# Kernel optimization log

Measured on AMD Instinct MI355X. Metric: run time of the kernel, lower is better.

Reference implementation:

```python
import jax, jax.numpy as jnp
import numpy as np

D = 1024      # num_embd
H = 16        # num_heads
HD = D // H   # head_size = 64
DFF = 4 * D
EPS = 1e-5


def layernorm(x, g, b):
    mu = jnp.mean(x, axis=-1, keepdims=True)
    var = jnp.mean((x - mu) ** 2, axis=-1, keepdims=True)
    return (x - mu) * jax.lax.rsqrt(var + EPS) * g + b


def setup_inputs() -> dict:
    key = jax.random.key(0)
    ks = jax.random.split(key, 12)
    B, S = 2, 2048
    s = lambda d: 1.0 / np.sqrt(d)
    return {
        "x": jax.random.normal(ks[0], (B, S, D), jnp.float32),
        "Wq": jax.random.normal(ks[1], (H, D, HD), jnp.float32) * s(D),
        "Wk": jax.random.normal(ks[2], (H, D, HD), jnp.float32) * s(D),
        "Wv": jax.random.normal(ks[3], (H, D, HD), jnp.float32) * s(D),
        "Wp": jax.random.normal(ks[4], (D, D), jnp.float32) * s(D),
        "bp": jnp.zeros((D,), jnp.float32),
        "W1": jax.random.normal(ks[5], (D, DFF), jnp.float32) * s(D),
        "b1": jnp.zeros((DFF,), jnp.float32),
        "W2": jax.random.normal(ks[6], (DFF, D), jnp.float32) * s(DFF),
        "b2": jnp.zeros((D,), jnp.float32),
        "g1": jnp.ones((D,), jnp.float32),
        "beta1": jnp.zeros((D,), jnp.float32),
        "g2": jnp.ones((D,), jnp.float32),
        "beta2": jnp.zeros((D,), jnp.float32),
    }


def reference(x, Wq, Wk, Wv, Wp, bp, W1, b1, W2, b2, g1, beta1, g2, beta2):
    B, S, _ = x.shape
    # --- self-attention with pre-LN residual ---
    h = layernorm(x, g1, beta1)
    q = jnp.einsum('bsd,hdk->bhsk', h, Wq)
    k = jnp.einsum('bsd,hdk->bhsk', h, Wk)
    v = jnp.einsum('bsd,hdk->bhsk', h, Wv)
    scores = jnp.einsum('bhqk,bhsk->bhqs', q, k) * (HD ** -0.5)
    causal = jnp.tril(jnp.ones((S, S), bool))
    scores = jnp.where(causal, scores, -jnp.inf)
    att = jax.nn.softmax(scores, axis=-1)          # dropout=0.0 (eval)
    o = jnp.einsum('bhqs,bhsk->bhqk', att, v)
    o = o.transpose(0, 2, 1, 3).reshape(B, S, D)   # concat heads
    x = x + o @ Wp + bp
    # --- feed-forward with pre-LN residual ---
    h2 = layernorm(x, g2, beta2)
    x = x + jax.nn.relu(h2 @ W1 + b1) @ W2 + b2
    return x
```

## Files before the change

### kernel.cpp

```cpp
#include <hip/hip_runtime.h>
#include <math.h>

#define DMODEL 1024
#define NHEAD  16
#define HD     64
#define DFF    4096
#define SEQ    2048
#define BATCH  2
#define NTOK   (BATCH * SEQ)
#define LN_EPS 1e-5f

typedef __attribute__((ext_vector_type(8))) short short8;
typedef __attribute__((ext_vector_type(4))) float floatx4;
typedef __attribute__((ext_vector_type(4))) unsigned short ushort4v;

__device__ __forceinline__ unsigned short f2bf(float x) {
  unsigned int u = __float_as_uint(x);
  return (unsigned short)((u + 0x7FFFu + ((u >> 16) & 1u)) >> 16);
}
__device__ __forceinline__ float bf2f(unsigned short h) {
  return __uint_as_float(((unsigned int)h) << 16);
}
__device__ __forceinline__ void split2(float x, unsigned short& hi, unsigned short& lo) {
  hi = f2bf(x);
  lo = f2bf(x - bf2f(hi));
}

__global__ __launch_bounds__(256) void ln_split(
    const float* __restrict__ x, const float* __restrict__ g,
    const float* __restrict__ beta, short* __restrict__ ohi,
    short* __restrict__ olo) {
  int row = blockIdx.x;
  const float4* xr = (const float4*)(x + (size_t)row * DMODEL);
  float4 v = xr[threadIdx.x];
  float s  = v.x + v.y + v.z + v.w;
  float sq = v.x * v.x + v.y * v.y + v.z * v.z + v.w * v.w;
#pragma unroll
  for (int off = 1; off < 64; off <<= 1) {
    s  += __shfl_xor(s, off);
    sq += __shfl_xor(sq, off);
  }
  __shared__ float red_s[4], red_q[4];
  int wave = threadIdx.x >> 6, lane = threadIdx.x & 63;
  if (lane == 0) { red_s[wave] = s; red_q[wave] = sq; }
  __syncthreads();
  s  = red_s[0] + red_s[1] + red_s[2] + red_s[3];
  sq = red_q[0] + red_q[1] + red_q[2] + red_q[3];
  float mu  = s * (1.0f / DMODEL);
  float var = sq * (1.0f / DMODEL) - mu * mu;
  float r   = rsqrtf(var + LN_EPS);
  float4 gv = ((const float4*)g)[threadIdx.x];
  float4 bv = ((const float4*)beta)[threadIdx.x];
  float o0 = (v.x - mu) * r * gv.x + bv.x;
  float o1 = (v.y - mu) * r * gv.y + bv.y;
  float o2 = (v.z - mu) * r * gv.z + bv.z;
  float o3 = (v.w - mu) * r * gv.w + bv.w;
  ushort4v hi, lo;
  unsigned short h_, l_;
  split2(o0, h_, l_); hi.x = h_; lo.x = l_;
  split2(o1, h_, l_); hi.y = h_; lo.y = l_;
  split2(o2, h_, l_); hi.z = h_; lo.z = l_;
  split2(o3, h_, l_); hi.w = h_; lo.w = l_;
  size_t base = (size_t)row * DMODEL + threadIdx.x * 4;
  *(ushort4v*)(ohi + base) = hi;
  *(ushort4v*)(olo + base) = lo;
}

__global__ __launch_bounds__(256) void split_rows(
    const float* __restrict__ in, short* __restrict__ ohi,
    short* __restrict__ olo) {
  size_t i = ((size_t)blockIdx.x * 256 + threadIdx.x) * 4;
  float4 v = *(const float4*)(in + i);
  ushort4v hi, lo;
  unsigned short h_, l_;
  split2(v.x, h_, l_); hi.x = h_; lo.x = l_;
  split2(v.y, h_, l_); hi.y = h_; lo.y = l_;
  split2(v.z, h_, l_); hi.z = h_; lo.z = l_;
  split2(v.w, h_, l_); hi.w = h_; lo.w = l_;
  *(ushort4v*)(ohi + i) = hi;
  *(ushort4v*)(olo + i) = lo;
}

__global__ __launch_bounds__(256) void repack_qkvT(
    const float* __restrict__ Wq, const float* __restrict__ Wk,
    const float* __restrict__ Wv, short* __restrict__ ohi,
    short* __restrict__ olo) {
  int i = blockIdx.x * 256 + threadIdx.x;
  int col = i >> 10;
  int d   = i & 1023;
  int m   = col >> 10;
  int c   = col & 1023;
  const float* W = (m == 0) ? Wq : (m == 1 ? Wk : Wv);
  int hh = c >> 6, kk = c & 63;
  float w = W[((size_t)hh * DMODEL + d) * HD + kk];
  unsigned short h_, l_;
  split2(w, h_, l_);
  ohi[i] = (short)h_;
  olo[i] = (short)l_;
}

__global__ __launch_bounds__(256) void transpose_split(
    const float* __restrict__ in, short* __restrict__ ohi,
    short* __restrict__ olo, int lgR, int C) {
  int i = blockIdx.x * 256 + threadIdx.x;
  int R = 1 << lgR;
  int oc = i >> lgR;
  int orow = i & (R - 1);
  float w = in[(size_t)orow * C + oc];
  unsigned short h_, l_;
  split2(w, h_, l_);
  ohi[i] = (short)h_;
  olo[i] = (short)l_;
}

template <int MODE>
__global__ __launch_bounds__(256) void gemm_mfma(
    const short* __restrict__ Ahi, const short* __restrict__ Alo,
    const short* __restrict__ Bhi, const short* __restrict__ Blo,
    const float* __restrict__ bias, const float* __restrict__ res,
    float* __restrict__ Cf, short* __restrict__ Chi, short* __restrict__ Clo,
    int M, int N, int K) {
  __shared__ short As[2][128][40];
  __shared__ short Bs[2][128][40];
  int tid = threadIdx.x;
  int wv = tid >> 6, lane = tid & 63;
  int wr = (wv >> 1) * 64;
  int wc = (wv & 1) * 64;
  int m0 = blockIdx.y * 128, n0 = blockIdx.x * 128;

  int srow = tid >> 1;
  int soff = (tid & 1) * 16;
  const short* pAh = Ahi + (size_t)(m0 + srow) * K + soff;
  const short* pAl = Alo + (size_t)(m0 + srow) * K + soff;
  const short* pBh = Bhi + (size_t)(n0 + srow) * K + soff;
  const short* pBl = Blo + (size_t)(n0 + srow) * K + soff;

  int fr = lane & 15;
  int ko = (lane >> 4) * 8;

  floatx4 acc[4][4];
#pragma unroll
  for (int i = 0; i < 4; i++)
#pragma unroll
    for (int j = 0; j < 4; j++) acc[i][j] = (floatx4){0.f, 0.f, 0.f, 0.f};

  for (int k0 = 0; k0 < K; k0 += 32) {
    short8 ga0 = *(const short8*)(pAh + k0);
    short8 ga1 = *(const short8*)(pAh + k0 + 8);
    short8 gb0 = *(const short8*)(pAl + k0);
    short8 gb1 = *(const short8*)(pAl + k0 + 8);
    short8 gc0 = *(const short8*)(pBh + k0);
    short8 gc1 = *(const short8*)(pBh + k0 + 8);
    short8 gd0 = *(const short8*)(pBl + k0);
    short8 gd1 = *(const short8*)(pBl + k0 + 8);
    __syncthreads();
    *(short8*)&As[0][srow][soff]     = ga0;
    *(short8*)&As[0][srow][soff + 8] = ga1;
    *(short8*)&As[1][srow][soff]     = gb0;
    *(short8*)&As[1][srow][soff + 8] = gb1;
    *(short8*)&Bs[0][srow][soff]     = gc0;
    *(short8*)&Bs[0][srow][soff + 8] = gc1;
    *(short8*)&Bs[1][srow][soff]     = gd0;
    *(short8*)&Bs[1][srow][soff + 8] = gd1;
    __syncthreads();

    short8 ah[4], al[4], bh[4], bl[4];
#pragma unroll
    for (int i = 0; i < 4; i++) {
      ah[i] = *(const short8*)&As[0][wr + i * 16 + fr][ko];
      al[i] = *(const short8*)&As[1][wr + i * 16 + fr][ko];
      bh[i] = *(const short8*)&Bs[0][wc + i * 16 + fr][ko];
      bl[i] = *(const short8*)&Bs[1][wc + i * 16 + fr][ko];
    }
#pragma unroll
    for (int i = 0; i < 4; i++)
#pragma unroll
      for (int j = 0; j < 4; j++) {
        acc[i][j] = __builtin_amdgcn_mfma_f32_16x16x32_bf16(ah[i], bh[j], acc[i][j], 0, 0, 0);
        acc[i][j] = __builtin_amdgcn_mfma_f32_16x16x32_bf16(ah[i], bl[j], acc[i][j], 0, 0, 0);
        acc[i][j] = __builtin_amdgcn_mfma_f32_16x16x32_bf16(al[i], bh[j], acc[i][j], 0, 0, 0);
      }
  }

  int r4 = (lane >> 4) * 4;
#pragma unroll
  for (int i = 0; i < 4; i++)
#pragma unroll
    for (int j = 0; j < 4; j++)
#pragma unroll
      for (int r = 0; r < 4; r++) {
        int row = m0 + wr + i * 16 + r4 + r;
        int col = n0 + wc + j * 16 + fr;
        float v = acc[i][j][r];
        if (MODE == 0) {
          Cf[(size_t)row * N + col] = v;
        } else if (MODE == 1) {
          Cf[(size_t)row * N + col] = v + bias[col] + res[(size_t)row * N + col];
        } else {
          v = fmaxf(v + bias[col], 0.f);
          unsigned short h_, l_;
          split2(v, h_, l_);
          Chi[(size_t)row * N + col] = (short)h_;
          Clo[(size_t)row * N + col] = (short)l_;
        }
      }
}

#define KT2 32
__global__ __launch_bounds__(256) void attn_mfma(
    const float* __restrict__ qkv, float* __restrict__ out) {
  int qb = blockIdx.x, h = blockIdx.y, b = blockIdx.z;
  int tid = threadIdx.x;
  int wv = tid >> 6, lane = tid & 63;
  int lr = lane & 15;
  int lg = lane >> 4;

  __shared__ short P_hi[4][16][40];
  __shared__ short P_lo[4][16][40];

  int q0 = qb * 64 + wv * 16;

  short8 qh[2], ql[2];
  {
    const float* qp = qkv + (size_t)(b * SEQ + q0 + lr) * 3072 + h * HD + lg * 8;
#pragma unroll
    for (int dc = 0; dc < 2; dc++) {
      float4 a = *(const float4*)(qp + dc * 32);
      float4 c = *(const float4*)(qp + dc * 32 + 4);
      float vals[8] = {a.x, a.y, a.z, a.w, c.x, c.y, c.z, c.w};
#pragma unroll
      for (int j = 0; j < 8; j++) {
        unsigned short h_, l_;
        split2(vals[j] * 0.125f, h_, l_);
        qh[dc][j] = (short)h_;
        ql[dc][j] = (short)l_;
      }
    }
  }

  floatx4 o_acc[4];
#pragma unroll
  for (int df = 0; df < 4; df++) o_acc[df] = (floatx4){0.f, 0.f, 0.f, 0.f};
  float m_st[4] = {-1e30f, -1e30f, -1e30f, -1e30f};
  float l_st[4] = {0.f, 0.f, 0.f, 0.f};

  const float* kbase = qkv + (size_t)(b * SEQ) * 3072 + 1024 + h * HD;
  const float* vbase = qkv + (size_t)(b * SEQ) * 3072 + 2048 + h * HD;

  int ntiles = (q0 + 15) / KT2 + 1;

  for (int t = 0; t < ntiles; t++) {
    int k0 = t * KT2;

    short8 kh[2][2], kl[2][2];
#pragma unroll
    for (int kf = 0; kf < 2; kf++) {
      const float* kp = kbase + (size_t)(k0 + kf * 16 + lr) * 3072 + lg * 8;
#pragma unroll
      for (int dc = 0; dc < 2; dc++) {
        float4 a = *(const float4*)(kp + dc * 32);
        float4 c = *(const float4*)(kp + dc * 32 + 4);
        float vals[8] = {a.x, a.y, a.z, a.w, c.x, c.y, c.z, c.w};
#pragma unroll
        for (int j = 0; j < 8; j++) {
          unsigned short h_, l_;
          split2(vals[j], h_, l_);
          kh[kf][dc][j] = (short)h_;
          kl[kf][dc][j] = (short)l_;
        }
      }
    }

    floatx4 s[2];
#pragma unroll
    for (int kf = 0; kf < 2; kf++) {
      floatx4 acc = (floatx4){0.f, 0.f, 0.f, 0.f};
#pragma unroll
      for (int dc = 0; dc < 2; dc++) {
        acc = __builtin_amdgcn_mfma_f32_16x16x32_bf16(qh[dc], kh[kf][dc], acc, 0, 0, 0);
        acc = __builtin_amdgcn_mfma_f32_16x16x32_bf16(qh[dc], kl[kf][dc], acc, 0, 0, 0);
        acc = __builtin_amdgcn_mfma_f32_16x16x32_bf16(ql[dc], kh[kf][dc], acc, 0, 0, 0);
      }
      s[kf] = acc;
    }

    float tmax[4];
#pragma unroll
    for (int r = 0; r < 4; r++) {
      int qg = q0 + lg * 4 + r;
#pragma unroll
      for (int kf = 0; kf < 2; kf++)
        if (k0 + kf * 16 + lr > qg) s[kf][r] = -3.0e38f;
      tmax[r] = fmaxf(s[0][r], s[1][r]);
    }
#pragma unroll
    for (int off = 1; off < 16; off <<= 1)
#pragma unroll
      for (int r = 0; r < 4; r++)
        tmax[r] = fmaxf(tmax[r], __shfl_xor(tmax[r], off));

    float p0[4], p1[4];
#pragma unroll
    for (int r = 0; r < 4; r++) {
      float mn = fmaxf(m_st[r], tmax[r]);
      float sc = __expf(m_st[r] - mn);
      m_st[r] = mn;
      p0[r] = __expf(s[0][r] - mn);
      p1[r] = __expf(s[1][r] - mn);
      l_st[r] = l_st[r] * sc + p0[r] + p1[r];
#pragma unroll
      for (int df = 0; df < 4; df++) o_acc[df][r] *= sc;
    }

#pragma unroll
    for (int r = 0; r < 4; r++) {
      unsigned short h_, l_;
      split2(p0[r], h_, l_);
      P_hi[wv][lg * 4 + r][lr] = (short)h_;
      P_lo[wv][lg * 4 + r][lr] = (short)l_;
      split2(p1[r], h_, l_);
      P_hi[wv][lg * 4 + r][16 + lr] = (short)h_;
      P_lo[wv][lg * 4 + r][16 + lr] = (short)l_;
    }
    short8 ph = *(const short8*)&P_hi[wv][lr][lg * 8];
    short8 pl = *(const short8*)&P_lo[wv][lr][lg * 8];

#pragma unroll
    for (int df = 0; df < 4; df++) {
      const float* vp = vbase + (size_t)(k0 + lg * 8) * 3072 + df * 16 + lr;
      float vals[8];
#pragma unroll
      for (int j = 0; j < 8; j++) vals[j] = vp[(size_t)j * 3072];
      short8 vh, vl;
#pragma unroll
      for (int j = 0; j < 8; j++) {
        unsigned short h_, l_;
        split2(vals[j], h_, l_);
        vh[j] = (short)h_;
        vl[j] = (short)l_;
      }
      o_acc[df] = __builtin_amdgcn_mfma_f32_16x16x32_bf16(ph, vh, o_acc[df], 0, 0, 0);
      o_acc[df] = __builtin_amdgcn_mfma_f32_16x16x32_bf16(ph, vl, o_acc[df], 0, 0, 0);
      o_acc[df] = __builtin_amdgcn_mfma_f32_16x16x32_bf16(pl, vh, o_acc[df], 0, 0, 0);
    }
  }

#pragma unroll
  for (int off = 1; off < 16; off <<= 1)
#pragma unroll
    for (int r = 0; r < 4; r++)
      l_st[r] += __shfl_xor(l_st[r], off);

#pragma unroll
  for (int r = 0; r < 4; r++) {
    float inv = 1.f / l_st[r];
    float* op = out + (size_t)(b * SEQ + q0 + lg * 4 + r) * DMODEL + h * HD;
#pragma unroll
    for (int df = 0; df < 4; df++)
      op[df * 16 + lr] = o_acc[df][r] * inv;
  }
}

extern "C" void kernel_launch(void* const* d_in, const int* in_sizes, int n_in,
                              void* d_out, int out_size, void* d_ws, size_t ws_size,
                              hipStream_t stream) {
  const float* x     = (const float*)d_in[0];
  const float* Wq    = (const float*)d_in[1];
  const float* Wk    = (const float*)d_in[2];
  const float* Wv    = (const float*)d_in[3];
  const float* Wp    = (const float*)d_in[4];
  const float* bp    = (const float*)d_in[5];
  const float* W1    = (const float*)d_in[6];
  const float* b1    = (const float*)d_in[7];
  const float* W2    = (const float*)d_in[8];
  const float* b2    = (const float*)d_in[9];
  const float* g1    = (const float*)d_in[10];
  const float* beta1 = (const float*)d_in[11];
  const float* g2    = (const float*)d_in[12];
  const float* beta2 = (const float*)d_in[13];
  float* out = (float*)d_out;

  char* ws = (char*)d_ws;
  short* h_hi     = (short*)(ws + 0);
  short* h_lo     = (short*)(ws + 8388608);
  short* WcT_hi   = (short*)(ws + 16777216);
  short* WcT_lo   = (short*)(ws + 23068672);
  float* qkv      = (float*)(ws + 29360128);
  float* attno    = (float*)(ws + 0);
  short* at_hi    = (short*)(ws + 16777216);
  short* at_lo    = (short*)(ws + 25165824);
  short* WpT_hi   = (short*)(ws + 33554432);
  short* WpT_lo   = (short*)(ws + 35651584);
  short* h2_hi    = (short*)(ws + 0);
  short* h2_lo    = (short*)(ws + 8388608);
  short* W1T_hi   = (short*)(ws + 16777216);
  short* W1T_lo   = (short*)(ws + 25165824);
  short* ffn_hi   = (short*)(ws + 33554432);
  short* ffn_lo   = (short*)(ws + 67108864);
  short* W2T_hi   = (short*)(ws + 0);
  short* W2T_lo   = (short*)(ws + 8388608);
  float* x1       = out;

  ln_split<<<NTOK, 256, 0, stream>>>(x, g1, beta1, h_hi, h_lo);
  repack_qkvT<<<(3072 * 1024) / 256, 256, 0, stream>>>(Wq, Wk, Wv, WcT_hi, WcT_lo);
  gemm_mfma<0><<<dim3(3072 / 128, NTOK / 128), 256, 0, stream>>>(
      h_hi, h_lo, WcT_hi, WcT_lo, nullptr, nullptr, qkv, nullptr, nullptr,
      NTOK, 3072, DMODEL);
  attn_mfma<<<dim3(SEQ / 64, NHEAD, BATCH), 256, 0, stream>>>(qkv, attno);
  split_rows<<<(NTOK * DMODEL) / 1024, 256, 0, stream>>>(attno, at_hi, at_lo);
  transpose_split<<<(1024 * 1024) / 256, 256, 0, stream>>>(Wp, WpT_hi, WpT_lo, 10, DMODEL);
  gemm_mfma<1><<<dim3(DMODEL / 128, NTOK / 128), 256, 0, stream>>>(
      at_hi, at_lo, WpT_hi, WpT_lo, bp, x, x1, nullptr, nullptr,
      NTOK, DMODEL, DMODEL);
  ln_split<<<NTOK, 256, 0, stream>>>(x1, g2, beta2, h2_hi, h2_lo);
  transpose_split<<<(1024 * 4096) / 256, 256, 0, stream>>>(W1, W1T_hi, W1T_lo, 10, DFF);
  gemm_mfma<2><<<dim3(DFF / 128, NTOK / 128), 256, 0, stream>>>(
      h2_hi, h2_lo, W1T_hi, W1T_lo, b1, nullptr, nullptr, ffn_hi, ffn_lo,
      NTOK, DFF, DMODEL);
  transpose_split<<<(4096 * 1024) / 256, 256, 0, stream>>>(W2, W2T_hi, W2T_lo, 12, DMODEL);
  gemm_mfma<1><<<dim3(DMODEL / 128, NTOK / 128), 256, 0, stream>>>(
      ffn_hi, ffn_lo, W2T_hi, W2T_lo, b2, x1, out, nullptr, nullptr,
      NTOK, DMODEL, DFF);
}
```

Before: 1.023 ms.

## Emit split bf16 QKV from GEMM, pre-transpose V, reverse attention block order

The QKV GEMM now writes hi/lo bf16 pairs directly instead of fp32, so attention no longer re-splits Q, K and V on every tile. A new kernel transposes V per head into a sequence-contiguous layout, letting the PV step use vector loads instead of strided scalar gathers. The query scale moves to the score accumulator, and query blocks are launched in reverse so the longest causal blocks start first. The cost is an extra transpose kernel and more workspace, and the Q scaling point changes slightly numerically.

```diff
diff --git a/kernel.cpp b/kernel.cpp
--- a/kernel.cpp
+++ b/kernel.cpp
@@ -113,6 +113,42 @@
   olo[i] = (short)l_;
 }
 
+__global__ __launch_bounds__(256) void vt_transpose(
+    const short* __restrict__ qkvh, const short* __restrict__ qkvl,
+    short* __restrict__ vth, short* __restrict__ vtl) {
+  int st = blockIdx.x;
+  int h = blockIdx.y, b = blockIdx.z;
+  __shared__ short Th[64][72];
+  __shared__ short Tl[64][72];
+  int tid = threadIdx.x;
+  {
+    int sl = tid >> 2, d0 = (tid & 3) * 16;
+    const short* ph = qkvh + (size_t)(b * SEQ + st * 64 + sl) * 3072 + 2048 + h * HD + d0;
+    const short* pl = qkvl + (size_t)(b * SEQ + st * 64 + sl) * 3072 + 2048 + h * HD + d0;
+    *(short8*)&Th[sl][d0]     = *(const short8*)ph;
+    *(short8*)&Th[sl][d0 + 8] = *(const short8*)(ph + 8);
+    *(short8*)&Tl[sl][d0]     = *(const short8*)pl;
+    *(short8*)&Tl[sl][d0 + 8] = *(const short8*)(pl + 8);
+  }
+  __syncthreads();
+  {
+    int dl = tid >> 2, s0 = (tid & 3) * 16;
+    short8 oh0, oh1, ol0, ol1;
+#pragma unroll
+    for (int j = 0; j < 8; j++) {
+      oh0[j] = Th[s0 + j][dl];
+      oh1[j] = Th[s0 + 8 + j][dl];
+      ol0[j] = Tl[s0 + j][dl];
+      ol1[j] = Tl[s0 + 8 + j][dl];
+    }
+    size_t obase = ((size_t)((b * NHEAD + h) * HD + dl)) * SEQ + st * 64 + s0;
+    *(short8*)(vth + obase)     = oh0;
+    *(short8*)(vth + obase + 8) = oh1;
+    *(short8*)(vtl + obase)     = ol0;
+    *(short8*)(vtl + obase + 8) = ol1;
+  }
+}
+
 template <int MODE>
 __global__ __launch_bounds__(256) void gemm_mfma(
     const short* __restrict__ Ahi, const short* __restrict__ Alo,
@@ -196,8 +232,13 @@
           Cf[(size_t)row * N + col] = v;
         } else if (MODE == 1) {
           Cf[(size_t)row * N + col] = v + bias[col] + res[(size_t)row * N + col];
+        } else if (MODE == 2) {
+          v = fmaxf(v + bias[col], 0.f);
+          unsigned short h_, l_;
+          split2(v, h_, l_);
+          Chi[(size_t)row * N + col] = (short)h_;
+          Clo[(size_t)row * N + col] = (short)l_;
         } else {
-          v = fmaxf(v + bias[col], 0.f);
           unsigned short h_, l_;
           split2(v, h_, l_);
           Chi[(size_t)row * N + col] = (short)h_;
@@ -208,8 +249,11 @@
 
 #define KT2 32
 __global__ __launch_bounds__(256) void attn_mfma(
-    const float* __restrict__ qkv, float* __restrict__ out) {
-  int qb = blockIdx.x, h = blockIdx.y, b = blockIdx.z;
+    const short* __restrict__ qkvh, const short* __restrict__ qkvl,
+    const short* __restrict__ vth, const short* __restrict__ vtl,
+    float* __restrict__ out) {
+  int qb = gridDim.x - 1 - blockIdx.x;
+  int h = blockIdx.y, b = blockIdx.z;
   int tid = threadIdx.x;
   int wv = tid >> 6, lane = tid & 63;
   int lr = lane & 15;
@@ -222,20 +266,12 @@
 
   short8 qh[2], ql[2];
   {
-    const float* qp = qkv + (size_t)(b * SEQ + q0 + lr) * 3072 + h * HD + lg * 8;
-#pragma unroll
-    for (int dc = 0; dc < 2; dc++) {
-      float4 a = *(const float4*)(qp + dc * 32);
-      float4 c = *(const float4*)(qp + dc * 32 + 4);
-      float vals[8] = {a.x, a.y, a.z, a.w, c.x, c.y, c.z, c.w};
-#pragma unroll
-      for (int j = 0; j < 8; j++) {
-        unsigned short h_, l_;
-        split2(vals[j] * 0.125f, h_, l_);
-        qh[dc][j] = (short)h_;
-        ql[dc][j] = (short)l_;
-      }
-    }
+    const short* qp  = qkvh + (size_t)(b * SEQ + q0 + lr) * 3072 + h * HD + lg * 8;
+    const short* qpl = qkvl + (size_t)(b * SEQ + q0 + lr) * 3072 + h * HD + lg * 8;
+    qh[0] = *(const short8*)qp;
+    qh[1] = *(const short8*)(qp + 32);
+    ql[0] = *(const short8*)qpl;
+    ql[1] = *(const short8*)(qpl + 32);
   }
 
   floatx4 o_acc[4];
@@ -244,8 +280,10 @@
   float m_st[4] = {-1e30f, -1e30f, -1e30f, -1e30f};
   float l_st[4] = {0.f, 0.f, 0.f, 0.f};
 
-  const float* kbase = qkv + (size_t)(b * SEQ) * 3072 + 1024 + h * HD;
-  const float* vbase = qkv + (size_t)(b * SEQ) * 3072 + 2048 + h * HD;
+  const short* kbh = qkvh + (size_t)(b * SEQ) * 3072 + 1024 + h * HD + lg * 8;
+  const short* kbl = qkvl + (size_t)(b * SEQ) * 3072 + 1024 + h * HD + lg * 8;
+  const short* vbh = vth + ((size_t)((b * NHEAD + h) * HD)) * SEQ;
+  const short* vbl = vtl + ((size_t)((b * NHEAD + h) * HD)) * SEQ;
 
   int ntiles = (q0 + 15) / KT2 + 1;
 
@@ -255,20 +293,12 @@
     short8 kh[2][2], kl[2][2];
 #pragma unroll
     for (int kf = 0; kf < 2; kf++) {
-      const float* kp = kbase + (size_t)(k0 + kf * 16 + lr) * 3072 + lg * 8;
-#pragma unroll
-      for (int dc = 0; dc < 2; dc++) {
-        float4 a = *(const float4*)(kp + dc * 32);
-        float4 c = *(const float4*)(kp + dc * 32 + 4);
-        float vals[8] = {a.x, a.y, a.z, a.w, c.x, c.y, c.z, c.w};
-#pragma unroll
-        for (int j = 0; j < 8; j++) {
-          unsigned short h_, l_;
-          split2(vals[j], h_, l_);
-          kh[kf][dc][j] = (short)h_;
-          kl[kf][dc][j] = (short)l_;
-        }
-      }
+      const short* kp  = kbh + (size_t)(k0 + kf * 16 + lr) * 3072;
+      const short* kpl = kbl + (size_t)(k0 + kf * 16 + lr) * 3072;
+      kh[kf][0] = *(const short8*)kp;
+      kh[kf][1] = *(const short8*)(kp + 32);
+      kl[kf][0] = *(const short8*)kpl;
+      kl[kf][1] = *(const short8*)(kpl + 32);
     }
 
     floatx4 s[2];
@@ -289,8 +319,10 @@
     for (int r = 0; r < 4; r++) {
       int qg = q0 + lg * 4 + r;
 #pragma unroll
-      for (int kf = 0; kf < 2; kf++)
+      for (int kf = 0; kf < 2; kf++) {
+        s[kf][r] *= 0.125f;
         if (k0 + kf * 16 + lr > qg) s[kf][r] = -3.0e38f;
+      }
       tmax[r] = fmaxf(s[0][r], s[1][r]);
     }
 #pragma unroll
@@ -327,18 +359,10 @@
 
 #pragma unroll
     for (int df = 0; df < 4; df++) {
-      const float* vp = vbase + (size_t)(k0 + lg * 8) * 3072 + df * 16 + lr;
-      float vals[8];
-#pragma unroll
-      for (int j = 0; j < 8; j++) vals[j] = vp[(size_t)j * 3072];
-      short8 vh, vl;
-#pragma unroll
-      for (int j = 0; j < 8; j++) {
-        unsigned short h_, l_;
-        split2(vals[j], h_, l_);
-        vh[j] = (short)h_;
-        vl[j] = (short)l_;
-      }
+      const short* vp  = vbh + (size_t)(df * 16 + lr) * SEQ + k0 + lg * 8;
+      const short* vpl = vbl + (size_t)(df * 16 + lr) * SEQ + k0 + lg * 8;
+      short8 vh = *(const short8*)vp;
+      short8 vl = *(const short8*)vpl;
       o_acc[df] = __builtin_amdgcn_mfma_f32_16x16x32_bf16(ph, vh, o_acc[df], 0, 0, 0);
       o_acc[df] = __builtin_amdgcn_mfma_f32_16x16x32_bf16(ph, vl, o_acc[df], 0, 0, 0);
       o_acc[df] = __builtin_amdgcn_mfma_f32_16x16x32_bf16(pl, vh, o_acc[df], 0, 0, 0);
@@ -385,7 +409,10 @@
   short* h_lo     = (short*)(ws + 8388608);
   short* WcT_hi   = (short*)(ws + 16777216);
   short* WcT_lo   = (short*)(ws + 23068672);
-  float* qkv      = (float*)(ws + 29360128);
+  short* qkvh     = (short*)(ws + 29360128);
+  short* qkvl     = (short*)(ws + 54525952);
+  short* vth      = (short*)(ws + 79691776);
+  short* vtl      = (short*)(ws + 88080384);
   float* attno    = (float*)(ws + 0);
   short* at_hi    = (short*)(ws + 16777216);
   short* at_lo    = (short*)(ws + 25165824);
@@ -403,10 +430,11 @@
 
   ln_split<<<NTOK, 256, 0, stream>>>(x, g1, beta1, h_hi, h_lo);
   repack_qkvT<<<(3072 * 1024) / 256, 256, 0, stream>>>(Wq, Wk, Wv, WcT_hi, WcT_lo);
-  gemm_mfma<0><<<dim3(3072 / 128, NTOK / 128), 256, 0, stream>>>(
-      h_hi, h_lo, WcT_hi, WcT_lo, nullptr, nullptr, qkv, nullptr, nullptr,
+  gemm_mfma<3><<<dim3(3072 / 128, NTOK / 128), 256, 0, stream>>>(
+      h_hi, h_lo, WcT_hi, WcT_lo, nullptr, nullptr, nullptr, qkvh, qkvl,
       NTOK, 3072, DMODEL);
-  attn_mfma<<<dim3(SEQ / 64, NHEAD, BATCH), 256, 0, stream>>>(qkv, attno);
+  vt_transpose<<<dim3(SEQ / 64, NHEAD, BATCH), 256, 0, stream>>>(qkvh, qkvl, vth, vtl);
+  attn_mfma<<<dim3(SEQ / 64, NHEAD, BATCH), 256, 0, stream>>>(qkvh, qkvl, vth, vtl, attno);
   split_rows<<<(NTOK * DMODEL) / 1024, 256, 0, stream>>>(attno, at_hi, at_lo);
   transpose_split<<<(1024 * 1024) / 256, 256, 0, stream>>>(Wp, WpT_hi, WpT_lo, 10, DMODEL);
   gemm_mfma<1><<<dim3(DMODEL / 128, NTOK / 128), 256, 0, stream>>>(
```

Result: slower. 1.120 ms (+9.5%).
